# Kernel optimization log

Measured on AMD Instinct MI355X. Metric: run time of the kernel, lower is better.

Reference implementation:

```python
import jax, jax.numpy as jnp
import numpy as np

# e2m1 (nvfp4) representable magnitudes and rounding midpoints
E2M1_POS = jnp.array([0.0, 0.5, 1.0, 1.5, 2.0, 3.0, 4.0, 6.0], dtype=jnp.float32)
E2M1_BOUNDS = jnp.array([0.25, 0.75, 1.25, 1.75, 2.5, 3.5, 5.0], dtype=jnp.float32)
E2M1_TABLE = jnp.concatenate([E2M1_POS, -E2M1_POS])  # 4-bit code -> value (sign bit = bit 3)
BLOCK = 16  # nvfp4 block-scale group size


def _fp8_round(v):
    # simulate storage of block scales in float8 e4m3
    return v.astype(jnp.float8_e4m3fn).astype(jnp.float32)


def _e2m1_round(v):
    # round-to-nearest onto the e2m1 grid (|v| must be pre-clipped to <= 6)
    idx = jnp.searchsorted(E2M1_BOUNDS, jnp.abs(v))
    return jnp.sign(v) * E2M1_POS[idx]


def setup_inputs() -> dict:
    key = jax.random.key(0)
    k1, k2, k3, k4, k5 = jax.random.split(key, 5)
    M, H = 4096, 4096
    x = jax.random.normal(k1, (M, 2 * H), dtype=jnp.float32)
    w = jax.random.randint(k2, (H, H // 2), 0, 256, dtype=jnp.int32)  # packed fp4, 2 nibbles/byte
    wscale = jax.random.normal(k3, (H, H // BLOCK), dtype=jnp.float32)  # cast to fp8 inside
    wscale2 = jax.random.uniform(k4, (1,), dtype=jnp.float32)
    scale = jax.random.uniform(k5, (1,), dtype=jnp.float32)
    return {"x": x, "w": w, "wscale": wscale, "wscale2": wscale2, "scale": scale}


def reference(x, w, wscale, wscale2, scale):
    M = x.shape[0]
    H = x.shape[1] // 2
    # SiLU-and-mul
    y = jax.nn.silu(x[:, :H]) * x[:, H:]                 # [M, H]
    gs = 1.0 / scale[0]                                  # global input scale (1/self.scale)
    # NVFP4 dynamic quant: per-16-element block amax -> fp8 block scale, values -> e2m1
    yb = y.reshape(M, H // BLOCK, BLOCK)
    amax = jnp.max(jnp.abs(yb), axis=-1)                 # [M, H/16]
    sf = _fp8_round(amax * (gs / 6.0))                   # fp8-stored block scales
    inv = jnp.where(sf > 0, gs / sf, 0.0)
    q = _e2m1_round(jnp.clip(yb * inv[..., None], -6.0, 6.0))
    a_deq = (q * sf[..., None]).reshape(M, H)            # fp4 value * fp8 block scale
    # Weight side: unpack fp4 nibbles (low nibble = even k), dequant with fp8 block scales
    wu = w.astype(jnp.uint8)
    lo = (wu & 0xF).astype(jnp.int32)
    hi = (wu >> 4).astype(jnp.int32)
    codes = jnp.stack([lo, hi], axis=-1).reshape(H, H)   # [N, K]
    b_q = E2M1_TABLE[codes]
    ws = _fp8_round(wscale)                              # model stores wscale in fp8
    b_deq = b_q * jnp.repeat(ws, BLOCK, axis=1)          # [N, K]
    # cutlass_scaled_fp4_mm with alpha = scale * wscale2 undoing global scales
    alpha = scale[0] * wscale2[0]
    out = alpha * (a_deq @ b_deq.T)                      # [M, N]
    return out
```

## Files before the change

### kernel.cpp

```cpp
#include <hip/hip_runtime.h>
#include <math.h>

typedef unsigned int uint;
typedef unsigned short ushort;
typedef __attribute__((ext_vector_type(8))) short bf16x8;
typedef __attribute__((ext_vector_type(4))) float f32x4;

static constexpr int Mdim = 4096;
static constexpr int Ndim = 4096;
static constexpr int Kdim = 4096;
static constexpr int Hdim = 4096;


__device__ __forceinline__ float fp8_round(float v) {
  float a = fabsf(v);
  float q;
  if (a >= 0x1p-6f) {
    uint u = __float_as_uint(a);
    int e = (int)(u >> 23) - 127;
    float quant = __uint_as_float((uint)(e - 3 + 127) << 23);
    q = rintf(a / quant) * quant;
    q = fminf(q, 448.f);
  } else {
    q = rintf(a * 512.f) * 0x1p-9f;
  }
  return copysignf(q, v);
}

__device__ __forceinline__ float e2m1_round(float t) {
  float a = fabsf(t);
  float q;
  if (a <= 0.25f) q = 0.f;
  else if (a <= 0.75f) q = 0.5f;
  else if (a <= 1.25f) q = 1.f;
  else if (a <= 1.75f) q = 1.5f;
  else if (a <= 2.5f)  q = 2.f;
  else if (a <= 3.5f)  q = 3.f;
  else if (a <= 5.f)   q = 4.f;
  else                 q = 6.f;
  return copysignf(q, t);
}

__device__ __forceinline__ float e2m1_decode(uint c) {
  uint m = c & 7u;
  float v;
  if (m == 0u) v = 0.f;
  else if (m == 1u) v = 0.5f;
  else v = __uint_as_float(((126u + (m >> 1)) << 23) | ((m & 1u) << 22));
  return (c & 8u) ? -v : v;
}


__global__ void prep_kernel(const float* __restrict__ x, const int* __restrict__ w,
                            const float* __restrict__ wscale,
                            const float* __restrict__ scalep,
                            ushort* __restrict__ a_deq, ushort* __restrict__ b_deq) {
  const int b = blockIdx.x;
  if (b < Mdim) {
    const int row = b;
    const int blk = threadIdx.x;
    const float gs = 1.0f / scalep[0];
    const float c6 = gs / 6.0f;
    const float* gp = x + (size_t)row * (2 * Hdim) + blk * 16;
    const float* up = gp + Hdim;
    float y[16];
    float amax = 0.f;
#pragma unroll
    for (int i = 0; i < 4; ++i) {
      float4 gv = ((const float4*)gp)[i];
      float4 uv = ((const float4*)up)[i];
      float ga[4] = {gv.x, gv.y, gv.z, gv.w};
      float ua[4] = {uv.x, uv.y, uv.z, uv.w};
#pragma unroll
      for (int j = 0; j < 4; ++j) {
        float xv = ga[j];
        float sig = 1.0f / (1.0f + expf(-xv));
        float yy = xv * sig * ua[j];
        y[i * 4 + j] = yy;
        amax = fmaxf(amax, fabsf(yy));
      }
    }
    const float sf = fp8_round(amax * c6);
    uint outp[8];
    if (sf > 0.f) {
      const float inv = gs / sf;
#pragma unroll
      for (int i = 0; i < 8; ++i) {
        float t0 = fminf(fmaxf(y[2 * i] * inv, -6.f), 6.f);
        float t1 = fminf(fmaxf(y[2 * i + 1] * inv, -6.f), 6.f);
        float d0 = e2m1_round(t0) * sf;
        float d1 = e2m1_round(t1) * sf;
        outp[i] = (__float_as_uint(d0) >> 16) | ((__float_as_uint(d1) >> 16) << 16);
      }
    } else {
#pragma unroll
      for (int i = 0; i < 8; ++i) outp[i] = 0u;
    }
    uint4* dst = (uint4*)(a_deq + (size_t)row * Hdim + blk * 16);
    dst[0] = (uint4){outp[0], outp[1], outp[2], outp[3]};
    dst[1] = (uint4){outp[4], outp[5], outp[6], outp[7]};
  } else {
    const int n = b - Mdim;
    const int blk = threadIdx.x;
    const int4* wp = (const int4*)(w + (size_t)n * (Hdim / 2) + blk * 8);
    int4 w0 = wp[0], w1 = wp[1];
    int wb[8] = {w0.x, w0.y, w0.z, w0.w, w1.x, w1.y, w1.z, w1.w};
    const float ws = fp8_round(wscale[(size_t)n * (Hdim / 16) + blk]);
    uint outp[8];
#pragma unroll
    for (int i = 0; i < 8; ++i) {
      uint byte = (uint)wb[i] & 0xFFu;
      float vlo = e2m1_decode(byte & 15u) * ws;
      float vhi = e2m1_decode(byte >> 4) * ws;
      outp[i] = (__float_as_uint(vlo) >> 16) | ((__float_as_uint(vhi) >> 16) << 16);
    }
    uint4* dst = (uint4*)(b_deq + (size_t)n * Hdim + blk * 16);
    dst[0] = (uint4){outp[0], outp[1], outp[2], outp[3]};
    dst[1] = (uint4){outp[4], outp[5], outp[6], outp[7]};
  }
}


#define BM 256
#define BN 256
#define BK 64
#define NT (Kdim / BK)
#define TILE_E (256 * 64)

__device__ __forceinline__ void gload_lds16(const ushort* g, ushort* l) {
  __builtin_amdgcn_global_load_lds((const __attribute__((address_space(1))) void*)g,
                                   (__attribute__((address_space(3))) void*)l,
                                   16, 0, 0);
}

#define BAR()                                   \
  do {                                          \
    asm volatile("" ::: "memory");              \
    __builtin_amdgcn_s_barrier();               \
    asm volatile("" ::: "memory");              \
  } while (0)

__global__ __launch_bounds__(512, 2) void gemm256(const ushort* __restrict__ A,
                                                  const ushort* __restrict__ B,
                                                  float* __restrict__ C,
                                                  const float* __restrict__ scalep,
                                                  const float* __restrict__ wscale2p) {
  extern __shared__ __align__(16) ushort lds[];
  const int tid = threadIdx.x;
  const int wave = tid >> 6;
  const int lane = tid & 63;
  const int wm = wave >> 2;
  const int wn = wave & 3;
  const int fr = lane & 15;
  const int fq = lane >> 4;

  const int wg = blockIdx.x;
  const int swz = (wg & 7) * 32 + (wg >> 3);
  const int m0 = (swz >> 4) * BM;
  const int n0 = (swz & 15) * BN;

  f32x4 acc[8][4];
#pragma unroll
  for (int i = 0; i < 8; ++i)
#pragma unroll
    for (int j = 0; j < 4; ++j) acc[i][j] = (f32x4){0.f, 0.f, 0.f, 0.f};

  ushort* pA0 = lds;
  ushort* pA1 = lds + TILE_E;
  ushort* pA2 = lds + 2 * TILE_E;
  ushort* pB0 = lds + 3 * TILE_E;
  ushort* pB1 = lds + 4 * TILE_E;

  int goffA[4], goffB[4], loff[4];
#pragma unroll
  for (int h = 0; h < 2; ++h)
#pragma unroll
    for (int rr = 0; rr < 2; ++rr) {
      const int idx = h * 2 + rr;
      const int rowb = h * 128 + rr * 64 + wave * 8;
      const int trow = rowb + (lane >> 3);
      const int sc = (lane & 7) ^ (trow & 7);
      goffA[idx] = (m0 + trow) * Kdim + sc * 8;
      goffB[idx] = (n0 + trow) * Kdim + sc * 8;
      loff[idx] = rowb * 64;
    }

#define STAGE_A(h, kcol)                                                       \
  do {                                                                         \
    gload_lds16(A + (size_t)goffA[(h)*2 + 0] + (kcol), pA2 + loff[(h)*2 + 0]); \
    gload_lds16(A + (size_t)goffA[(h)*2 + 1] + (kcol), pA2 + loff[(h)*2 + 1]); \
  } while (0)
#define STAGE_B(h, kcol)                                                       \
  do {                                                                         \
    gload_lds16(B + (size_t)goffB[(h)*2 + 0] + (kcol), pB0 + loff[(h)*2 + 0]); \
    gload_lds16(B + (size_t)goffB[(h)*2 + 1] + (kcol), pB0 + loff[(h)*2 + 1]); \
  } while (0)

  const int laneAOff = (wm * 128 + fr) * 64;
  const int laneBOff = (wn * 64 + fr) * 64;
  const int xo0 = (fq ^ (fr & 7)) * 8;
  const int xo1 = ((4 + fq) ^ (fr & 7)) * 8;

  {
    ushort* sv = pA2;
    pA2 = pA0; STAGE_A(0, 0); STAGE_A(1, 0);
    STAGE_B(0, 0); STAGE_B(1, 0);
    pA2 = pA1; STAGE_A(0, BK); STAGE_A(1, BK);
    { ushort* t = pB0; pB0 = pB1; STAGE_B(0, BK); STAGE_B(1, BK); pB0 = t; }
    pA2 = sv;
  }
  asm volatile("s_waitcnt vmcnt(8)" ::: "memory");
  BAR();

  bf16x8 af0[2][2], bfr[4][2];
  {
    const ushort* aR0 = pA0 + laneAOff + xo0;
    const ushort* aR1 = pA0 + laneAOff + xo1;
    const ushort* bR0 = pB0 + laneBOff + xo0;
    const ushort* bR1 = pB0 + laneBOff + xo1;
#pragma unroll
    for (int ni = 0; ni < 4; ++ni) {
      bfr[ni][0] = *(const bf16x8*)(bR0 + ni * 1024);
      bfr[ni][1] = *(const bf16x8*)(bR1 + ni * 1024);
    }
#pragma unroll
    for (int m2 = 0; m2 < 2; ++m2) {
      af0[m2][0] = *(const bf16x8*)(aR0 + m2 * 1024);
      af0[m2][1] = *(const bf16x8*)(aR1 + m2 * 1024);
    }
  }

  for (int kt = 0; kt < NT; ++kt) {
    const int kc = (kt + 2) * BK;
    const bool stg = (kt + 2) < NT;
    const bool nxt = (kt + 1) < NT;
    const ushort* aR0 = pA0 + laneAOff + xo0;
    const ushort* aR1 = pA0 + laneAOff + xo1;
    bf16x8 af1[2][2], af2[2][2], af3[2][2];

#pragma unroll
    for (int m2 = 0; m2 < 2; ++m2) {
      af1[m2][0] = *(const bf16x8*)(aR0 + (2 + m2) * 1024);
      af1[m2][1] = *(const bf16x8*)(aR1 + (2 + m2) * 1024);
    }
    if (stg) STAGE_A(0, kc);
    __builtin_amdgcn_s_setprio(1);
#pragma unroll
    for (int m2 = 0; m2 < 2; ++m2)
#pragma unroll
      for (int ni = 0; ni < 4; ++ni)
#pragma unroll
        for (int kk = 0; kk < 2; ++kk)
          acc[m2][ni] = __builtin_amdgcn_mfma_f32_16x16x32_bf16(af0[m2][kk], bfr[ni][kk],
                                                                acc[m2][ni], 0, 0, 0);
    __builtin_amdgcn_s_setprio(0);
    BAR();

#pragma unroll
    for (int m2 = 0; m2 < 2; ++m2) {
      af2[m2][0] = *(const bf16x8*)(aR0 + (4 + m2) * 1024);
      af2[m2][1] = *(const bf16x8*)(aR1 + (4 + m2) * 1024);
    }
    if (stg) STAGE_A(1, kc);
    __builtin_amdgcn_s_setprio(1);
#pragma unroll
    for (int m2 = 0; m2 < 2; ++m2)
#pragma unroll
      for (int ni = 0; ni < 4; ++ni)
#pragma unroll
        for (int kk = 0; kk < 2; ++kk)
          acc[2 + m2][ni] = __builtin_amdgcn_mfma_f32_16x16x32_bf16(af1[m2][kk], bfr[ni][kk],
                                                                    acc[2 + m2][ni], 0, 0, 0);
    __builtin_amdgcn_s_setprio(0);
    BAR();

#pragma unroll
    for (int m2 = 0; m2 < 2; ++m2) {
      af3[m2][0] = *(const bf16x8*)(aR0 + (6 + m2) * 1024);
      af3[m2][1] = *(const bf16x8*)(aR1 + (6 + m2) * 1024);
    }
    if (stg) STAGE_B(0, kc);
    __builtin_amdgcn_s_setprio(1);
#pragma unroll
    for (int m2 = 0; m2 < 2; ++m2)
#pragma unroll
      for (int ni = 0; ni < 4; ++ni)
#pragma unroll
        for (int kk = 0; kk < 2; ++kk)
          acc[4 + m2][ni] = __builtin_amdgcn_mfma_f32_16x16x32_bf16(af2[m2][kk], bfr[ni][kk],
                                                                    acc[4 + m2][ni], 0, 0, 0);
    __builtin_amdgcn_s_setprio(0);
    if (stg) asm volatile("s_waitcnt vmcnt(6)" ::: "memory");
    else     asm volatile("s_waitcnt vmcnt(0)" ::: "memory");
    BAR();

    if (stg) STAGE_B(1, kc);
    __builtin_amdgcn_s_setprio(1);
#pragma unroll
    for (int m2 = 0; m2 < 2; ++m2)
#pragma unroll
      for (int ni = 0; ni < 4; ++ni)
#pragma unroll
        for (int kk = 0; kk < 2; ++kk)
          acc[6 + m2][ni] = __builtin_amdgcn_mfma_f32_16x16x32_bf16(af3[m2][kk], bfr[ni][kk],
                                                                    acc[6 + m2][ni], 0, 0, 0);
    __builtin_amdgcn_s_setprio(0);
    if (nxt) {
      const ushort* aN0 = pA1 + laneAOff + xo0;
      const ushort* aN1 = pA1 + laneAOff + xo1;
      const ushort* bN0 = pB1 + laneBOff + xo0;
      const ushort* bN1 = pB1 + laneBOff + xo1;
#pragma unroll
      for (int ni = 0; ni < 4; ++ni) {
        bfr[ni][0] = *(const bf16x8*)(bN0 + ni * 1024);
        bfr[ni][1] = *(const bf16x8*)(bN1 + ni * 1024);
      }
#pragma unroll
      for (int m2 = 0; m2 < 2; ++m2) {
        af0[m2][0] = *(const bf16x8*)(aN0 + m2 * 1024);
        af0[m2][1] = *(const bf16x8*)(aN1 + m2 * 1024);
      }
    }
    BAR();

    { ushort* t = pA0; pA0 = pA1; pA1 = pA2; pA2 = t; }
    { ushort* t = pB0; pB0 = pB1; pB1 = t; }
  }

  const float alpha = scalep[0] * wscale2p[0];
#pragma unroll
  for (int mi = 0; mi < 8; ++mi)
#pragma unroll
    for (int ni = 0; ni < 4; ++ni) {
      const int col = n0 + wn * 64 + ni * 16 + fr;
      const int rbase = m0 + wm * 128 + mi * 16 + fq * 4;
#pragma unroll
      for (int r = 0; r < 4; ++r)
        __builtin_nontemporal_store(alpha * acc[mi][ni][r],
                                    &C[(size_t)(rbase + r) * Ndim + col]);
    }
}


extern "C" void kernel_launch(void* const* d_in, const int* in_sizes, int n_in,
                              void* d_out, int out_size, void* d_ws, size_t ws_size,
                              hipStream_t stream) {
  const float* x       = (const float*)d_in[0];
  const int*   w       = (const int*)d_in[1];
  const float* wscale  = (const float*)d_in[2];
  const float* wscale2 = (const float*)d_in[3];
  const float* scale   = (const float*)d_in[4];
  float* out = (float*)d_out;

  ushort* a_deq = (ushort*)d_ws;
  ushort* b_deq = a_deq + (size_t)Mdim * Kdim;

  prep_kernel<<<Mdim + Ndim, 256, 0, stream>>>(x, w, wscale, scale, a_deq, b_deq);

  (void)hipFuncSetAttribute((const void*)gemm256, hipFuncAttributeMaxDynamicSharedMemorySize, 163840);
  gemm256<<<(Mdim / BM) * (Ndim / BN), 512, 163840, stream>>>(a_deq, b_deq, out, scale, wscale2);
}
```

Baseline: 149.8 us.

## Merge four MFMA phases per K-tile into two with fewer barriers

The GEMM main loop now runs two phases per K-tile instead of four. It preloads the af1 fragments alongside af0, issues both A-stage copies together and then both B-stage copies together, and interleaves two accumulator groups in each MFMA block. This drops two of the four block barriers per iteration and gives each wave larger MFMA runs between synchronisations. In exchange, more A fragments stay live in registers, which may cost occupancy. The vmcnt wait is also moved, and the next-tile LDS fragment reads now follow that wait with no barrier in between, which may risk reading LDS data that other waves have not finished staging.

```diff
diff --git a/kernel.cpp b/kernel.cpp
--- a/kernel.cpp
+++ b/kernel.cpp
@@ -212,7 +212,7 @@
   asm volatile("s_waitcnt vmcnt(8)" ::: "memory");
   BAR();
 
-  bf16x8 af0[2][2], bfr[4][2];
+  bf16x8 af0[2][2], af1[2][2], bfr[4][2];
   {
     const ushort* aR0 = pA0 + laneAOff + xo0;
     const ushort* aR1 = pA0 + laneAOff + xo1;
@@ -227,6 +227,8 @@
     for (int m2 = 0; m2 < 2; ++m2) {
       af0[m2][0] = *(const bf16x8*)(aR0 + m2 * 1024);
       af0[m2][1] = *(const bf16x8*)(aR1 + m2 * 1024);
+      af1[m2][0] = *(const bf16x8*)(aR0 + (2 + m2) * 1024);
+      af1[m2][1] = *(const bf16x8*)(aR1 + (2 + m2) * 1024);
     }
   }
 
@@ -236,75 +238,47 @@
     const bool nxt = (kt + 1) < NT;
     const ushort* aR0 = pA0 + laneAOff + xo0;
     const ushort* aR1 = pA0 + laneAOff + xo1;
-    bf16x8 af1[2][2], af2[2][2], af3[2][2];
-
-#pragma unroll
-    for (int m2 = 0; m2 < 2; ++m2) {
-      af1[m2][0] = *(const bf16x8*)(aR0 + (2 + m2) * 1024);
-      af1[m2][1] = *(const bf16x8*)(aR1 + (2 + m2) * 1024);
-    }
-    if (stg) STAGE_A(0, kc);
-    __builtin_amdgcn_s_setprio(1);
-#pragma unroll
-    for (int m2 = 0; m2 < 2; ++m2)
-#pragma unroll
-      for (int ni = 0; ni < 4; ++ni)
-#pragma unroll
-        for (int kk = 0; kk < 2; ++kk)
-          acc[m2][ni] = __builtin_amdgcn_mfma_f32_16x16x32_bf16(af0[m2][kk], bfr[ni][kk],
-                                                                acc[m2][ni], 0, 0, 0);
-    __builtin_amdgcn_s_setprio(0);
-    BAR();
+    bf16x8 af2[2][2], af3[2][2];
 
 #pragma unroll
     for (int m2 = 0; m2 < 2; ++m2) {
       af2[m2][0] = *(const bf16x8*)(aR0 + (4 + m2) * 1024);
       af2[m2][1] = *(const bf16x8*)(aR1 + (4 + m2) * 1024);
-    }
-    if (stg) STAGE_A(1, kc);
+      af3[m2][0] = *(const bf16x8*)(aR0 + (6 + m2) * 1024);
+      af3[m2][1] = *(const bf16x8*)(aR1 + (6 + m2) * 1024);
+    }
+    if (stg) { STAGE_A(0, kc); STAGE_A(1, kc); }
     __builtin_amdgcn_s_setprio(1);
 #pragma unroll
     for (int m2 = 0; m2 < 2; ++m2)
 #pragma unroll
       for (int ni = 0; ni < 4; ++ni)
 #pragma unroll
-        for (int kk = 0; kk < 2; ++kk)
+        for (int kk = 0; kk < 2; ++kk) {
+          acc[m2][ni] = __builtin_amdgcn_mfma_f32_16x16x32_bf16(af0[m2][kk], bfr[ni][kk],
+                                                                acc[m2][ni], 0, 0, 0);
           acc[2 + m2][ni] = __builtin_amdgcn_mfma_f32_16x16x32_bf16(af1[m2][kk], bfr[ni][kk],
                                                                     acc[2 + m2][ni], 0, 0, 0);
+        }
     __builtin_amdgcn_s_setprio(0);
     BAR();
 
-#pragma unroll
-    for (int m2 = 0; m2 < 2; ++m2) {
-      af3[m2][0] = *(const bf16x8*)(aR0 + (6 + m2) * 1024);
-      af3[m2][1] = *(const bf16x8*)(aR1 + (6 + m2) * 1024);
-    }
-    if (stg) STAGE_B(0, kc);
+    if (stg) { STAGE_B(0, kc); STAGE_B(1, kc); }
     __builtin_amdgcn_s_setprio(1);
 #pragma unroll
     for (int m2 = 0; m2 < 2; ++m2)
 #pragma unroll
       for (int ni = 0; ni < 4; ++ni)
 #pragma unroll
-        for (int kk = 0; kk < 2; ++kk)
+        for (int kk = 0; kk < 2; ++kk) {
           acc[4 + m2][ni] = __builtin_amdgcn_mfma_f32_16x16x32_bf16(af2[m2][kk], bfr[ni][kk],
                                                                     acc[4 + m2][ni], 0, 0, 0);
-    __builtin_amdgcn_s_setprio(0);
-    if (stg) asm volatile("s_waitcnt vmcnt(6)" ::: "memory");
-    else     asm volatile("s_waitcnt vmcnt(0)" ::: "memory");
-    BAR();
-
-    if (stg) STAGE_B(1, kc);
-    __builtin_amdgcn_s_setprio(1);
-#pragma unroll
-    for (int m2 = 0; m2 < 2; ++m2)
-#pragma unroll
-      for (int ni = 0; ni < 4; ++ni)
-#pragma unroll
-        for (int kk = 0; kk < 2; ++kk)
           acc[6 + m2][ni] = __builtin_amdgcn_mfma_f32_16x16x32_bf16(af3[m2][kk], bfr[ni][kk],
                                                                     acc[6 + m2][ni], 0, 0, 0);
+        }
     __builtin_amdgcn_s_setprio(0);
+    if (stg) asm volatile("s_waitcnt vmcnt(8)" ::: "memory");
+    else     asm volatile("s_waitcnt vmcnt(0)" ::: "memory");
     if (nxt) {
       const ushort* aN0 = pA1 + laneAOff + xo0;
       const ushort* aN1 = pA1 + laneAOff + xo1;
@@ -319,6 +293,8 @@
       for (int m2 = 0; m2 < 2; ++m2) {
         af0[m2][0] = *(const bf16x8*)(aN0 + m2 * 1024);
         af0[m2][1] = *(const bf16x8*)(aN1 + m2 * 1024);
+        af1[m2][0] = *(const bf16x8*)(aN0 + (2 + m2) * 1024);
+        af1[m2][1] = *(const bf16x8*)(aN1 + (2 + m2) * 1024);
       }
     }
     BAR();
```

After: 150.1 us (median of 2 runs). About the same (+0.2%).
